# Optimization experiments

Measured on AMD Instinct MI355X. Metric: run time of the kernel, lower is better.

Reference implementation:

```python
import jax, jax.numpy as jnp
import numpy as np

EPS = 1e-5  # BatchNorm eps

def _bn(x):
    # BatchNorm1d(affine=False) in training mode: per-agent, per-feature batch stats
    m = jnp.mean(x, axis=1, keepdims=True)
    v = jnp.var(x, axis=1, keepdims=True)
    return (x - m) / jnp.sqrt(v + EPS)

def _lrelu(x):
    return jax.nn.leaky_relu(x, 0.01)

def setup_inputs() -> dict:
    key = jax.random.key(0)
    ks = jax.random.split(key, 14)
    A, B, IN, OUT, H, K = 8, 32768, 128, 32, 128, 4
    D = H // K
    s = 0.05
    return {
        "states": jax.random.normal(ks[0], (A, B, IN), jnp.float32),
        "actions": jax.random.normal(ks[1], (A, B, OUT), jnp.float32),
        "enc_w": jax.random.normal(ks[2], (A, IN + OUT, H), jnp.float32) * s,
        "enc_b": jax.random.normal(ks[3], (A, H), jnp.float32) * s,
        "aenc_w": jax.random.normal(ks[4], (A, OUT, H), jnp.float32) * s,
        "aenc_b": jax.random.normal(ks[5], (A, H), jnp.float32) * s,
        "key_w": jax.random.normal(ks[6], (K, H, D), jnp.float32) * s,
        "sel_w": jax.random.normal(ks[7], (K, H, D), jnp.float32) * s,
        "val_w": jax.random.normal(ks[8], (K, H, D), jnp.float32) * s,
        "val_b": jax.random.normal(ks[9], (K, D), jnp.float32) * s,
        "c1_w": jax.random.normal(ks[10], (A, 2 * H, H), jnp.float32) * s,
        "c1_b": jax.random.normal(ks[11], (A, H), jnp.float32) * s,
        "c2_w": jax.random.normal(ks[12], (A, H, 1), jnp.float32) * s,
        "c2_b": jax.random.normal(ks[13], (A, 1), jnp.float32) * s,
    }

def reference(states, actions, enc_w, enc_b, aenc_w, aenc_b,
              key_w, sel_w, val_w, val_b, c1_w, c1_b, c2_w, c2_b):
    A, B, _ = states.shape
    # per-agent state-action encodings: [A,B,H]
    sa = _bn(jnp.concatenate([states, actions], axis=-1))
    sa_enc = _lrelu(jnp.einsum('abi,aih->abh', sa, enc_w) + enc_b[:, None, :])
    # per-agent action encodings: [A,B,H]
    a_in = _bn(actions)
    a_enc = _lrelu(jnp.einsum('abi,aih->abh', a_in, aenc_w) + aenc_b[:, None, :])
    # per-head keys/values/selectors: [K,A,B,D]
    keys = jnp.einsum('abh,khd->kabd', a_enc, key_w)
    vals = _lrelu(jnp.einsum('abh,khd->kabd', a_enc, val_w) + val_b[:, None, None, :])
    sels = jnp.einsum('abh,khd->kabd', sa_enc, sel_w)
    D = keys.shape[-1]
    # attention logits over other agents: [K,B,A_query,A_key], self excluded
    logits = jnp.einsum('kibd,kjbd->kbij', sels, keys) / jnp.sqrt(jnp.float32(D))
    self_mask = jnp.eye(A, dtype=bool)[None, None]
    probs = jax.nn.softmax(jnp.where(self_mask, -jnp.inf, logits), axis=-1)
    # attended values: [K,A,B,D] -> concat heads -> [A,B,K*D]
    other = jnp.einsum('kbij,kjbd->kibd', probs, vals)
    other_cat = jnp.transpose(other, (1, 2, 0, 3)).reshape(A, B, -1)
    # per-agent critics on [sa_enc, attended]: [A,B,1]
    critic_in = jnp.concatenate([sa_enc, other_cat], axis=-1)
    h = _lrelu(jnp.einsum('abi,aih->abh', critic_in, c1_w) + c1_b[:, None, :])
    q = jnp.einsum('abh,aho->abo', h, c2_w) + c2_b[:, None, :]
    return q
```

## Files before the change

kernel.cpp:

```cpp
#include <hip/hip_runtime.h>
#include <hip/hip_bf16.h>
#include <stdint.h>

#define A_N 8
#define B_N 32768
#define IN_N 128
#define OUT_N 32
#define SAF 160
#define H_N 128
#define D_N 32
#define KD_N 128
#define CIN_N 256
#define CHUNKS 128
#define EPSV 1e-5f
#define ENC_KP 192

typedef unsigned int u32;
typedef unsigned short u16;
typedef __attribute__((ext_vector_type(8))) short short8;
typedef __attribute__((ext_vector_type(4))) float floatx4;

__device__ __forceinline__ float bf_lo(u32 u){ return __uint_as_float(u << 16); }
__device__ __forceinline__ float bf_hi(u32 u){ return __uint_as_float(u & 0xffff0000u); }
__device__ __forceinline__ float bf2f(u16 b){ return __uint_as_float(((u32)b) << 16); }
__device__ __forceinline__ u16 f2bf(float f){
  u32 u = __float_as_uint(f);
  return (u16)((u + 0x7fffu + ((u >> 16) & 1u)) >> 16);
}
__device__ __forceinline__ float lrelu(float x){ return x > 0.f ? x : 0.01f * x; }

__global__ __launch_bounds__(256) void k_stats(
    const float* __restrict__ states, const float* __restrict__ actions,
    float* __restrict__ part)
{
  int a = blockIdx.y;
  int chunk = blockIdx.x;
  int t = threadIdx.x;
  int r0 = chunk * (B_N / CHUNKS);
  __shared__ float red[512];
  {
    int f = t & 127, half = t >> 7;
    const float* p = states + ((size_t)a * B_N + r0 + half) * IN_N + f;
    float s1 = 0.f, s2 = 0.f;
    for (int it = 0; it < 128; ++it){
      float v = p[(size_t)(2 * it) * IN_N];
      s1 += v; s2 += v * v;
    }
    red[t] = s1; red[256 + t] = s2;
    __syncthreads();
    if (t < 128){
      float a1 = red[t] + red[t + 128];
      float a2 = red[256 + t] + red[256 + t + 128];
      size_t o = (((size_t)a * CHUNKS + chunk) * SAF + t) * 2;
      part[o] = a1; part[o + 1] = a2;
    }
    __syncthreads();
  }
  {
    int f = t & 31, g = t >> 5;
    const float* p = actions + ((size_t)a * B_N + r0 + g) * OUT_N + f;
    float s1 = 0.f, s2 = 0.f;
    for (int it = 0; it < 32; ++it){
      float v = p[(size_t)(8 * it) * OUT_N];
      s1 += v; s2 += v * v;
    }
    red[t] = s1; red[256 + t] = s2;
    __syncthreads();
    if (t < 32){
      float a1 = 0.f, a2 = 0.f;
      #pragma unroll
      for (int gg = 0; gg < 8; ++gg){
        a1 += red[t + 32 * gg];
        a2 += red[256 + t + 32 * gg];
      }
      size_t o = (((size_t)a * CHUNKS + chunk) * SAF + 128 + t) * 2;
      part[o] = a1; part[o + 1] = a2;
    }
  }
}

__global__ void k_finalize(const float* __restrict__ part,
                           float* __restrict__ meanArr, float* __restrict__ istdArr)
{
  int idx = blockIdx.x * blockDim.x + threadIdx.x;
  if (idx >= A_N * SAF) return;
  int a = idx / SAF, f = idx % SAF;
  float s1 = 0.f, s2 = 0.f;
  for (int c = 0; c < CHUNKS; ++c){
    size_t o = (((size_t)a * CHUNKS + c) * SAF + f) * 2;
    s1 += part[o]; s2 += part[o + 1];
  }
  float m = s1 * (1.f / B_N);
  float v = s2 * (1.f / B_N) - m * m;
  if (v < 0.f) v = 0.f;
  meanArr[idx] = m;
  istdArr[idx] = rsqrtf(v + EPSV);
}

__device__ __forceinline__ void packpair(float w, u16* __restrict__ dh,
                                         u16* __restrict__ dl, int i){
  u16 h = f2bf(w);
  dh[i] = h;
  dl[i] = f2bf(w - bf2f(h));
}

__global__ __launch_bounds__(256) void k_pack(
    const float* __restrict__ enc_w, const float* __restrict__ aenc_w,
    const float* __restrict__ key_w, const float* __restrict__ sel_w,
    const float* __restrict__ val_w, const float* __restrict__ c1_w,
    u16* __restrict__ encH, u16* __restrict__ encL,
    u16* __restrict__ aencH, u16* __restrict__ aencL,
    u16* __restrict__ keyH, u16* __restrict__ keyL,
    u16* __restrict__ selH, u16* __restrict__ selL,
    u16* __restrict__ valH, u16* __restrict__ valL,
    u16* __restrict__ c1H, u16* __restrict__ c1L)
{
  int i = blockIdx.x * 256 + threadIdx.x;
  const int S0 = A_N * H_N * ENC_KP;
  const int S1 = A_N * H_N * OUT_N;
  const int S2 = KD_N * H_N;
  const int S5 = A_N * H_N * CIN_N;
  if (i < S0){
    int a = i / (H_N * ENC_KP); int r = i % (H_N * ENC_KP);
    int n = r / ENC_KP; int k = r % ENC_KP;
    float v = (k < SAF) ? enc_w[((size_t)a * SAF + k) * H_N + n] : 0.f;
    packpair(v, encH, encL, i);
    return;
  }
  i -= S0;
  if (i < S1){
    int a = i / (H_N * OUT_N); int r = i % (H_N * OUT_N);
    int n = r / OUT_N; int k = r % OUT_N;
    packpair(aenc_w[((size_t)a * OUT_N + k) * H_N + n], aencH, aencL, i);
    return;
  }
  i -= S1;
  if (i < 3 * S2){
    int which = i / S2; int j = i % S2;
    int n = j / H_N, k = j % H_N;
    const float* w = (which == 0) ? key_w : ((which == 1) ? sel_w : val_w);
    u16* dh = (which == 0) ? keyH : ((which == 1) ? selH : valH);
    u16* dl = (which == 0) ? keyL : ((which == 1) ? selL : valL);
    packpair(w[(((size_t)(n >> 5)) * H_N + k) * D_N + (n & 31)], dh, dl, j);
    return;
  }
  i -= 3 * S2;
  if (i < S5){
    int a = i / (H_N * CIN_N); int r = i % (H_N * CIN_N);
    int n = r / CIN_N; int k = r % CIN_N;
    packpair(c1_w[((size_t)a * CIN_N + k) * H_N + n], c1H, c1L, i);
  }
}
#define PACK_TOTAL (A_N*H_N*ENC_KP + A_N*H_N*OUT_N + 3*KD_N*H_N + A_N*H_N*CIN_N)

__global__ __launch_bounds__(256, 2) void k_enc_sel(
    const float* __restrict__ states, const float* __restrict__ actions,
    const float* __restrict__ mean, const float* __restrict__ istd,
    const u16* __restrict__ encH, const u16* __restrict__ encL,
    const float* __restrict__ enc_b,
    const u16* __restrict__ selH, const u16* __restrict__ selL,
    u16* __restrict__ sa_enc, u16* __restrict__ sels)
{
  int a = blockIdx.y; int row0 = blockIdx.x * 128; int t = threadIdx.x;
  int lane = t & 63, wave = t >> 6, l16 = lane & 15, quad = lane >> 4;
  __shared__ __align__(16) u16 WA[18432];
  __shared__ __align__(16) u16 XA[18432];
  __shared__ __align__(16) float sc[192], sh[192];
  u16* Wh = WA; u16* Wl = WA + 9216;
  u16* Xh = XA; u16* Xl = XA + 9216;
  u16* T  = XA;

  if (t < 192){
    float m = 0.f, s = 0.f;
    if (t < SAF){ m = mean[a * SAF + t]; s = istd[a * SAF + t]; }
    sc[t] = s; sh[t] = -m * s;
  }
  floatx4 acc[2][8];
  #pragma unroll
  for (int mt = 0; mt < 2; ++mt)
    #pragma unroll
    for (int nt = 0; nt < 8; ++nt) acc[mt][nt] = (floatx4){0.f,0.f,0.f,0.f};
  const u16* wbh = encH + (size_t)a * H_N * ENC_KP;
  const u16* wbl = encL + (size_t)a * H_N * ENC_KP;
  __syncthreads();

  for (int k0 = 0; k0 < ENC_KP; k0 += 64){
    for (int c = t; c < 1024; c += 256){
      int n = c >> 3, off = (c & 7) * 8;
      *(uint4*)&Wh[n * 72 + off] = *(const uint4*)(wbh + (size_t)n * ENC_KP + k0 + off);
      *(uint4*)&Wl[n * 72 + off] = *(const uint4*)(wbl + (size_t)n * ENC_KP + k0 + off);
    }
    for (int c = t; c < 2048; c += 256){
      int r = c >> 4, kc = (c & 15) * 4, f = k0 + kc;
      size_t row = (size_t)a * B_N + row0 + r;
      float4 v = {0.f, 0.f, 0.f, 0.f};
      if (f < IN_N)     v = *(const float4*)(states + row * IN_N + f);
      else if (f < SAF) v = *(const float4*)(actions + row * OUT_N + (f - IN_N));
      float4 scv = *(const float4*)&sc[f];
      float4 shv = *(const float4*)&sh[f];
      float x0 = fmaf(v.x, scv.x, shv.x), x1 = fmaf(v.y, scv.y, shv.y);
      float x2 = fmaf(v.z, scv.z, shv.z), x3 = fmaf(v.w, scv.w, shv.w);
      u16 h0 = f2bf(x0), h1 = f2bf(x1), h2 = f2bf(x2), h3 = f2bf(x3);
      *(u32*)&Xh[r * 72 + kc]     = (u32)h0 | ((u32)h1 << 16);
      *(u32*)&Xh[r * 72 + kc + 2] = (u32)h2 | ((u32)h3 << 16);
      u16 l0 = f2bf(x0 - bf2f(h0)), l1 = f2bf(x1 - bf2f(h1));
      u16 l2 = f2bf(x2 - bf2f(h2)), l3 = f2bf(x3 - bf2f(h3));
      *(u32*)&Xl[r * 72 + kc]     = (u32)l0 | ((u32)l1 << 16);
      *(u32*)&Xl[r * 72 + kc + 2] = (u32)l2 | ((u32)l3 << 16);
    }
    __syncthreads();
    #pragma unroll
    for (int ks = 0; ks < 64; ks += 32){
      short8 ah[2], al[2], bh[8], bl[8];
      #pragma unroll
      for (int mt = 0; mt < 2; ++mt){
        int rr = (wave * 32 + mt * 16 + l16) * 72 + ks + quad * 8;
        ah[mt] = *(const short8*)&Xh[rr];
        al[mt] = *(const short8*)&Xl[rr];
      }
      #pragma unroll
      for (int nt = 0; nt < 8; ++nt){
        int rr = (nt * 16 + l16) * 72 + ks + quad * 8;
        bh[nt] = *(const short8*)&Wh[rr];
        bl[nt] = *(const short8*)&Wl[rr];
      }
      #pragma unroll
      for (int mt = 0; mt < 2; ++mt)
        #pragma unroll
        for (int nt = 0; nt < 8; ++nt){
          acc[mt][nt] = __builtin_amdgcn_mfma_f32_16x16x32_bf16(ah[mt], bh[nt], acc[mt][nt], 0,0,0);
          acc[mt][nt] = __builtin_amdgcn_mfma_f32_16x16x32_bf16(ah[mt], bl[nt], acc[mt][nt], 0,0,0);
          acc[mt][nt] = __builtin_amdgcn_mfma_f32_16x16x32_bf16(al[mt], bh[nt], acc[mt][nt], 0,0,0);
        }
    }
    __syncthreads();
  }

  {
    float bv[8];
    #pragma unroll
    for (int nt = 0; nt < 8; ++nt) bv[nt] = enc_b[a * H_N + nt * 16 + l16];
    #pragma unroll
    for (int mt = 0; mt < 2; ++mt)
      #pragma unroll
      for (int nt = 0; nt < 8; ++nt)
        #pragma unroll
        for (int r = 0; r < 4; ++r){
          int rl = wave * 32 + mt * 16 + quad * 4 + r;
          T[rl * 136 + nt * 16 + l16] = f2bf(lrelu(acc[mt][nt][r] + bv[nt]));
        }
  }
  __syncthreads();
  for (int c = t; c < 2048; c += 256){
    int row = c >> 4, col8 = (c & 15) * 8;
    *(uint4*)(sa_enc + ((size_t)a * B_N + row0 + row) * H_N + col8) =
        *(const uint4*)&T[row * 136 + col8];
  }

  #pragma unroll
  for (int mt = 0; mt < 2; ++mt)
    #pragma unroll
    for (int nt = 0; nt < 8; ++nt) acc[mt][nt] = (floatx4){0.f,0.f,0.f,0.f};
  for (int k0 = 0; k0 < H_N; k0 += 64){
    __syncthreads();
    for (int c = t; c < 1024; c += 256){
      int n = c >> 3, off = (c & 7) * 8;
      *(uint4*)&Wh[n * 72 + off] = *(const uint4*)(selH + (size_t)n * H_N + k0 + off);
      *(uint4*)&Wl[n * 72 + off] = *(const uint4*)(selL + (size_t)n * H_N + k0 + off);
    }
    __syncthreads();
    #pragma unroll
    for (int ks = 0; ks < 64; ks += 32){
      short8 ah[2], bh[8], bl[8];
      #pragma unroll
      for (int mt = 0; mt < 2; ++mt)
        ah[mt] = *(const short8*)&T[(wave * 32 + mt * 16 + l16) * 136 + k0 + ks + quad * 8];
      #pragma unroll
      for (int nt = 0; nt < 8; ++nt){
        int rr = (nt * 16 + l16) * 72 + ks + quad * 8;
        bh[nt] = *(const short8*)&Wh[rr];
        bl[nt] = *(const short8*)&Wl[rr];
      }
      #pragma unroll
      for (int mt = 0; mt < 2; ++mt)
        #pragma unroll
        for (int nt = 0; nt < 8; ++nt){
          acc[mt][nt] = __builtin_amdgcn_mfma_f32_16x16x32_bf16(ah[mt], bh[nt], acc[mt][nt], 0,0,0);
          acc[mt][nt] = __builtin_amdgcn_mfma_f32_16x16x32_bf16(ah[mt], bl[nt], acc[mt][nt], 0,0,0);
        }
    }
  }
  __syncthreads();
  #pragma unroll
  for (int mt = 0; mt < 2; ++mt)
    #pragma unroll
    for (int nt = 0; nt < 8; ++nt)
      #pragma unroll
      for (int r = 0; r < 4; ++r){
        int rl = wave * 32 + mt * 16 + quad * 4 + r;
        T[rl * 136 + nt * 16 + l16] = f2bf(acc[mt][nt][r]);
      }
  __syncthreads();
  for (int c = t; c < 2048; c += 256){
    int row = c >> 4, col8 = (c & 15) * 8;
    *(uint4*)(sels + ((size_t)a * B_N + row0 + row) * H_N + col8) =
        *(const uint4*)&T[row * 136 + col8];
  }
}

__global__ __launch_bounds__(256, 2) void k_aenc_kv(
    const float* __restrict__ actions,
    const float* __restrict__ mean, const float* __restrict__ istd,
    const u16* __restrict__ aencH, const u16* __restrict__ aencL,
    const float* __restrict__ aenc_b,
    const u16* __restrict__ keyH, const u16* __restrict__ keyL,
    const u16* __restrict__ valH, const u16* __restrict__ valL,
    const float* __restrict__ val_b,
    u16* __restrict__ keys, u16* __restrict__ vals)
{
  int a = blockIdx.y; int row0 = blockIdx.x * 128; int t = threadIdx.x;
  int lane = t & 63, wave = t >> 6, l16 = lane & 15, quad = lane >> 4;
  __shared__ __align__(16) u16 WA[18432];
  __shared__ __align__(16) u16 TA[17408];
  __shared__ __align__(16) float sc[32], sh[32];
  u16* T = TA;

  if (t < 32){
    float m = mean[a * SAF + 128 + t], s = istd[a * SAF + 128 + t];
    sc[t] = s; sh[t] = -m * s;
  }
  floatx4 acc[2][8];
  #pragma unroll
  for (int mt = 0; mt < 2; ++mt)
    #pragma unroll
    for (int nt = 0; nt < 8; ++nt) acc[mt][nt] = (floatx4){0.f,0.f,0.f,0.f};
  __syncthreads();

  {
    u16* Xh = TA; u16* Xl = TA + 5120;
    u16* Wh1 = WA; u16* Wl1 = WA + 5120;
    const u16* wbh = aencH + (size_t)a * H_N * OUT_N;
    const u16* wbl = aencL + (size_t)a * H_N * OUT_N;
    for (int c = t; c < 512; c += 256){
      int n = c >> 2, off = (c & 3) * 8;
      *(uint4*)&Wh1[n * 40 + off] = *(const uint4*)(wbh + (size_t)n * OUT_N + off);
      *(uint4*)&Wl1[n * 40 + off] = *(const uint4*)(wbl + (size_t)n * OUT_N + off);
    }
    for (int c = t; c < 1024; c += 256){
      int r = c >> 3, kc = (c & 7) * 4;
      size_t row = (size_t)a * B_N + row0 + r;
      float4 v = *(const float4*)(actions + row * OUT_N + kc);
      float4 scv = *(const float4*)&sc[kc];
      float4 shv = *(const float4*)&sh[kc];
      float x0 = fmaf(v.x, scv.x, shv.x), x1 = fmaf(v.y, scv.y, shv.y);
      float x2 = fmaf(v.z, scv.z, shv.z), x3 = fmaf(v.w, scv.w, shv.w);
      u16 h0 = f2bf(x0), h1 = f2bf(x1), h2 = f2bf(x2), h3 = f2bf(x3);
      *(u32*)&Xh[r * 40 + kc]     = (u32)h0 | ((u32)h1 << 16);
      *(u32*)&Xh[r * 40 + kc + 2] = (u32)h2 | ((u32)h3 << 16);
      u16 l0 = f2bf(x0 - bf2f(h0)), l1 = f2bf(x1 - bf2f(h1));
      u16 l2 = f2bf(x2 - bf2f(h2)), l3 = f2bf(x3 - bf2f(h3));
      *(u32*)&Xl[r * 40 + kc]     = (u32)l0 | ((u32)l1 << 16);
      *(u32*)&Xl[r * 40 + kc + 2] = (u32)l2 | ((u32)l3 << 16);
    }
    __syncthreads();
    short8 ah[2], al[2], bh[8], bl[8];
    #pragma unroll
    for (int mt = 0; mt < 2; ++mt){
      int rr = (wave * 32 + mt * 16 + l16) * 40 + quad * 8;
      ah[mt] = *(const short8*)&Xh[rr];
      al[mt] = *(const short8*)&Xl[rr];
    }
    #pragma unroll
    for (int nt = 0; nt < 8; ++nt){
      int rr = (nt * 16 + l16) * 40 + quad * 8;
      bh[nt] = *(const short8*)&Wh1[rr];
      bl[nt] = *(const short8*)&Wl1[rr];
    }
    #pragma unroll
    for (int mt = 0; mt < 2; ++mt)
      #pragma unroll
      for (int nt = 0; nt < 8; ++nt){
        acc[mt][nt] = __builtin_amdgcn_mfma_f32_16x16x32_bf16(ah[mt], bh[nt], acc[mt][nt], 0,0,0);
        acc[mt][nt] = __builtin_amdgcn_mfma_f32_16x16x32_bf16(ah[mt], bl[nt], acc[mt][nt], 0,0,0);
        acc[mt][nt] = __builtin_amdgcn_mfma_f32_16x16x32_bf16(al[mt], bh[nt], acc[mt][nt], 0,0,0);
      }
    __syncthreads();
  }
  {
    float bv[8];
    #pragma unroll
    for (int nt = 0; nt < 8; ++nt) bv[nt] = aenc_b[a * H_N + nt * 16 + l16];
    #pragma unroll
    for (int mt = 0; mt < 2; ++mt)
      #pragma unroll
      for (int nt = 0; nt < 8; ++nt)
        #pragma unroll
        for (int r = 0; r < 4; ++r){
          int rl = wave * 32 + mt * 16 + quad * 4 + r;
          T[rl * 136 + nt * 16 + l16] = f2bf(lrelu(acc[mt][nt][r] + bv[nt]));
        }
  }

  u16* Wh = WA; u16* Wl = WA + 9216;
  #pragma unroll
  for (int mt = 0; mt < 2; ++mt)
    #pragma unroll
    for (int nt = 0; nt < 8; ++nt) acc[mt][nt] = (floatx4){0.f,0.f,0.f,0.f};
  for (int k0 = 0; k0 < H_N; k0 += 64){
    __syncthreads();
    for (int c = t; c < 1024; c += 256){
      int n = c >> 3, off = (c & 7) * 8;
      *(uint4*)&Wh[n * 72 + off] = *(const uint4*)(keyH + (size_t)n * H_N + k0 + off);
      *(uint4*)&Wl[n * 72 + off] = *(const uint4*)(keyL + (size_t)n * H_N + k0 + off);
    }
    __syncthreads();
    #pragma unroll
    for (int ks = 0; ks < 64; ks += 32){
      short8 ah[2], bh[8], bl[8];
      #pragma unroll
      for (int mt = 0; mt < 2; ++mt)
        ah[mt] = *(const short8*)&T[(wave * 32 + mt * 16 + l16) * 136 + k0 + ks + quad * 8];
      #pragma unroll
      for (int nt = 0; nt < 8; ++nt){
        int rr = (nt * 16 + l16) * 72 + ks + quad * 8;
        bh[nt] = *(const short8*)&Wh[rr];
        bl[nt] = *(const short8*)&Wl[rr];
      }
      #pragma unroll
      for (int mt = 0; mt < 2; ++mt)
        #pragma unroll
        for (int nt = 0; nt < 8; ++nt){
          acc[mt][nt] = __builtin_amdgcn_mfma_f32_16x16x32_bf16(ah[mt], bh[nt], acc[mt][nt], 0,0,0);
          acc[mt][nt] = __builtin_amdgcn_mfma_f32_16x16x32_bf16(ah[mt], bl[nt], acc[mt][nt], 0,0,0);
        }
    }
  }
  #pragma unroll
  for (int mt = 0; mt < 2; ++mt)
    #pragma unroll
    for (int nt = 0; nt < 8; ++nt)
      #pragma unroll
      for (int r = 0; r < 4; ++r){
        int rl = wave * 32 + mt * 16 + quad * 4 + r;
        keys[((size_t)a * B_N + row0 + rl) * H_N + nt * 16 + l16] = f2bf(acc[mt][nt][r]);
      }

  #pragma unroll
  for (int mt = 0; mt < 2; ++mt)
    #pragma unroll
    for (int nt = 0; nt < 8; ++nt) acc[mt][nt] = (floatx4){0.f,0.f,0.f,0.f};
  for (int k0 = 0; k0 < H_N; k0 += 64){
    __syncthreads();
    for (int c = t; c < 1024; c += 256){
      int n = c >> 3, off = (c & 7) * 8;
      *(uint4*)&Wh[n * 72 + off] = *(const uint4*)(valH + (size_t)n * H_N + k0 + off);
      *(uint4*)&Wl[n * 72 + off] = *(const uint4*)(valL + (size_t)n * H_N + k0 + off);
    }
    __syncthreads();
    #pragma unroll
    for (int ks = 0; ks < 64; ks += 32){
      short8 ah[2], bh[8], bl[8];
      #pragma unroll
      for (int mt = 0; mt < 2; ++mt)
        ah[mt] = *(const short8*)&T[(wave * 32 + mt * 16 + l16) * 136 + k0 + ks + quad * 8];
      #pragma unroll
      for (int nt = 0; nt < 8; ++nt){
        int rr = (nt * 16 + l16) * 72 + ks + quad * 8;
        bh[nt] = *(const short8*)&Wh[rr];
        bl[nt] = *(const short8*)&Wl[rr];
      }
      #pragma unroll
      for (int mt = 0; mt < 2; ++mt)
        #pragma unroll
        for (int nt = 0; nt < 8; ++nt){
          acc[mt][nt] = __builtin_amdgcn_mfma_f32_16x16x32_bf16(ah[mt], bh[nt], acc[mt][nt], 0,0,0);
          acc[mt][nt] = __builtin_amdgcn_mfma_f32_16x16x32_bf16(ah[mt], bl[nt], acc[mt][nt], 0,0,0);
        }
    }
  }
  __syncthreads();
  {
    float bv[8];
    #pragma unroll
    for (int nt = 0; nt < 8; ++nt) bv[nt] = val_b[nt * 16 + l16];
    #pragma unroll
    for (int mt = 0; mt < 2; ++mt)
      #pragma unroll
      for (int nt = 0; nt < 8; ++nt)
        #pragma unroll
        for (int r = 0; r < 4; ++r){
          int rl = wave * 32 + mt * 16 + quad * 4 + r;
          T[rl * 136 + nt * 16 + l16] = f2bf(lrelu(acc[mt][nt][r] + bv[nt]));
        }
  }
  __syncthreads();
  for (int c = t; c < 2048; c += 256){
    int row = c >> 4, col8 = (c & 15) * 8;
    *(uint4*)(vals + ((size_t)a * B_N + row0 + row) * H_N + col8) =
        *(const uint4*)&T[row * 136 + col8];
  }
}

__global__ __launch_bounds__(256) void k_attn(
    const u16* __restrict__ sels, const u16* __restrict__ keys,
    const u16* __restrict__ vals, u16* __restrict__ other)
{
  int b0 = blockIdx.x * 8;
  int t = threadIdx.x;
  __shared__ __align__(16) u16 sS[8192], sK[8192], sV[8192];
  u32* dS = (u32*)sS; u32* dK = (u32*)sK; u32* dV = (u32*)sV;
  #pragma unroll
  for (int a = 0; a < 8; ++a){
    size_t go = ((size_t)a * B_N + b0) * KD_N;
    const u32* gs = (const u32*)(sels + go);
    const u32* gk = (const u32*)(keys + go);
    const u32* gv = (const u32*)(vals + go);
    dS[a * 512 + t] = gs[t]; dS[a * 512 + 256 + t] = gs[256 + t];
    dK[a * 512 + t] = gk[t]; dK[a * 512 + 256 + t] = gk[256 + t];
    dV[a * 512 + t] = gv[t]; dV[a * 512 + 256 + t] = gv[256 + t];
  }
  __syncthreads();
  int i = t & 7, p = t >> 3;
  int k = p & 3, bl = p >> 2;
  int base_i = (i * 8 + bl) * 128 + k * 32;
  float si[32];
  {
    const u32* S32 = (const u32*)&sS[base_i];
    #pragma unroll
    for (int d2 = 0; d2 < 16; ++d2){
      u32 u = S32[d2];
      si[2 * d2] = bf_lo(u); si[2 * d2 + 1] = bf_hi(u);
    }
  }
  float lg[8];
  #pragma unroll
  for (int j = 0; j < 8; ++j){
    const u32* K32 = (const u32*)&sK[(j * 8 + bl) * 128 + k * 32];
    float acc = 0.f;
    #pragma unroll
    for (int d2 = 0; d2 < 16; ++d2){
      u32 u = K32[d2];
      acc = fmaf(si[2 * d2], bf_lo(u), acc);
      acc = fmaf(si[2 * d2 + 1], bf_hi(u), acc);
    }
    lg[j] = acc * 0.17677669529663689f;
  }
  float mx = -3.0e38f;
  #pragma unroll
  for (int j = 0; j < 8; ++j) if (j != i) mx = fmaxf(mx, lg[j]);
  float pe[8], se = 0.f;
  #pragma unroll
  for (int j = 0; j < 8; ++j){
    pe[j] = (j == i) ? 0.f : __expf(lg[j] - mx);
    se += pe[j];
  }
  float inv = 1.f / se;
  #pragma unroll
  for (int j = 0; j < 8; ++j) pe[j] *= inv;
  __align__(16) u16 ob[32];
  #pragma unroll
  for (int d2 = 0; d2 < 16; ++d2){
    float acc0 = 0.f, acc1 = 0.f;
    #pragma unroll
    for (int j = 0; j < 8; ++j){
      u32 u = *(const u32*)&sV[(j * 8 + bl) * 128 + k * 32 + 2 * d2];
      acc0 = fmaf(pe[j], bf_lo(u), acc0);
      acc1 = fmaf(pe[j], bf_hi(u), acc1);
    }
    ob[2 * d2] = f2bf(acc0); ob[2 * d2 + 1] = f2bf(acc1);
  }
  uint4* dst = (uint4*)(other + ((size_t)i * B_N + (b0 + bl)) * KD_N + k * 32);
  const uint4* s4 = (const uint4*)ob;
  #pragma unroll
  for (int c = 0; c < 4; ++c) dst[c] = s4[c];
}

__global__ __launch_bounds__(256, 2) void k_critic(
    const u16* __restrict__ sa_enc, const u16* __restrict__ other,
    const u16* __restrict__ c1H, const u16* __restrict__ c1L,
    const float* __restrict__ c1_b,
    const float* __restrict__ c2w, const float* __restrict__ c2b,
    float* __restrict__ qout)
{
  int a = blockIdx.y; int row0 = blockIdx.x * 128; int t = threadIdx.x;
  int lane = t & 63, wave = t >> 6, l16 = lane & 15, quad = lane >> 4;
  __shared__ __align__(16) u16 Xs[9216];
  __shared__ __align__(16) u16 Wh[9216];
  __shared__ __align__(16) u16 Wl[9216];
  floatx4 acc[2][8];
  #pragma unroll
  for (int mt = 0; mt < 2; ++mt)
    #pragma unroll
    for (int nt = 0; nt < 8; ++nt) acc[mt][nt] = (floatx4){0.f,0.f,0.f,0.f};
  const u16* wbh = c1H + (size_t)a * H_N * CIN_N;
  const u16* wbl = c1L + (size_t)a * H_N * CIN_N;

  for (int k0 = 0; k0 < CIN_N; k0 += 64){
    for (int c = t; c < 1024; c += 256){
      int n = c >> 3, off = (c & 7) * 8;
      *(uint4*)&Wh[n * 72 + off] = *(const uint4*)(wbh + (size_t)n * CIN_N + k0 + off);
      *(uint4*)&Wl[n * 72 + off] = *(const uint4*)(wbl + (size_t)n * CIN_N + k0 + off);
    }
    for (int c = t; c < 1024; c += 256){
      int r = c >> 3, off = (c & 7) * 8;
      int fo = k0 + off;
      const u16* src = sa_enc;
      if (fo >= H_N){ src = other; fo -= H_N; }
      *(uint4*)&Xs[r * 72 + off] =
          *(const uint4*)(src + ((size_t)a * B_N + row0 + r) * H_N + fo);
    }
    __syncthreads();
    #pragma unroll
    for (int ks = 0; ks < 64; ks += 32){
      short8 ah[2], bh[8], bl[8];
      #pragma unroll
      for (int mt = 0; mt < 2; ++mt)
        ah[mt] = *(const short8*)&Xs[(wave * 32 + mt * 16 + l16) * 72 + ks + quad * 8];
      #pragma unroll
      for (int nt = 0; nt < 8; ++nt){
        int rr = (nt * 16 + l16) * 72 + ks + quad * 8;
        bh[nt] = *(const short8*)&Wh[rr];
        bl[nt] = *(const short8*)&Wl[rr];
      }
      #pragma unroll
      for (int mt = 0; mt < 2; ++mt)
        #pragma unroll
        for (int nt = 0; nt < 8; ++nt){
          acc[mt][nt] = __builtin_amdgcn_mfma_f32_16x16x32_bf16(ah[mt], bh[nt], acc[mt][nt], 0,0,0);
          acc[mt][nt] = __builtin_amdgcn_mfma_f32_16x16x32_bf16(ah[mt], bl[nt], acc[mt][nt], 0,0,0);
        }
    }
    __syncthreads();
  }

  float c2r[8], bv[8];
  #pragma unroll
  for (int nt = 0; nt < 8; ++nt){
    c2r[nt] = c2w[a * H_N + nt * 16 + l16];
    bv[nt]  = c1_b[a * H_N + nt * 16 + l16];
  }
  #pragma unroll
  for (int mt = 0; mt < 2; ++mt){
    #pragma unroll
    for (int r = 0; r < 4; ++r){
      float s = 0.f;
      #pragma unroll
      for (int nt = 0; nt < 8; ++nt){
        float h = lrelu(acc[mt][nt][r] + bv[nt]);
        s = fmaf(h, c2r[nt], s);
      }
      s += __shfl_xor(s, 1);
      s += __shfl_xor(s, 2);
      s += __shfl_xor(s, 4);
      s += __shfl_xor(s, 8);
      if (l16 == 0){
        int row = row0 + wave * 32 + mt * 16 + quad * 4 + r;
        qout[(size_t)a * B_N + row] = s + c2b[a];
      }
    }
  }
}

extern "C" void kernel_launch(void* const* d_in, const int* in_sizes, int n_in,
                              void* d_out, int out_size, void* d_ws, size_t ws_size,
                              hipStream_t stream)
{
  const float* states  = (const float*)d_in[0];
  const float* actions = (const float*)d_in[1];
  const float* enc_w   = (const float*)d_in[2];
  const float* enc_b   = (const float*)d_in[3];
  const float* aenc_w  = (const float*)d_in[4];
  const float* aenc_b  = (const float*)d_in[5];
  const float* key_w   = (const float*)d_in[6];
  const float* sel_w   = (const float*)d_in[7];
  const float* val_w   = (const float*)d_in[8];
  const float* val_b   = (const float*)d_in[9];
  const float* c1_w    = (const float*)d_in[10];
  const float* c1_b    = (const float*)d_in[11];
  const float* c2_w    = (const float*)d_in[12];
  const float* c2_b    = (const float*)d_in[13];
  float* q = (float*)d_out;

  char* ws = (char*)d_ws;
  u16* encH  = (u16*)(ws + 0);
  u16* encL  = (u16*)(ws + 393216);
  u16* aencH = (u16*)(ws + 786432);
  u16* aencL = (u16*)(ws + 851968);
  u16* keyH  = (u16*)(ws + 917504);
  u16* keyL  = (u16*)(ws + 950272);
  u16* selH  = (u16*)(ws + 983040);
  u16* selL  = (u16*)(ws + 1015808);
  u16* valH  = (u16*)(ws + 1048576);
  u16* valL  = (u16*)(ws + 1081344);
  float* part    = (float*)ws;
  float* meanArr = (float*)(ws + 1310720);
  float* istdArr = (float*)(ws + 1315840);
  u16* c1H = (u16*)(ws + 1320960);
  u16* c1L = (u16*)(ws + 1845248);
  const size_t ibase = 4194304;
  const size_t BUF = (size_t)A_N * B_N * 128 * 2;
  u16* sa_enc = (u16*)(ws + ibase);
  u16* sels   = (u16*)(ws + ibase + BUF);
  u16* keys   = (u16*)(ws + ibase + 2 * BUF);
  u16* vals   = (u16*)(ws + ibase + 3 * BUF);

  k_stats<<<dim3(CHUNKS, A_N), 256, 0, stream>>>(states, actions, part);
  k_finalize<<<(A_N * SAF + 255) / 256, 256, 0, stream>>>(part, meanArr, istdArr);
  k_pack<<<(PACK_TOTAL + 255) / 256, 256, 0, stream>>>(
      enc_w, aenc_w, key_w, sel_w, val_w, c1_w,
      encH, encL, aencH, aencL, keyH, keyL, selH, selL, valH, valL, c1H, c1L);

  dim3 g(B_N / 128, A_N);
  k_enc_sel<<<g, 256, 0, stream>>>(states, actions, meanArr, istdArr,
                                   encH, encL, enc_b, selH, selL, sa_enc, sels);
  k_aenc_kv<<<g, 256, 0, stream>>>(actions, meanArr, istdArr,
                                   aencH, aencL, aenc_b, keyH, keyL,
                                   valH, valL, val_b, keys, vals);
  k_attn<<<B_N / 8, 256, 0, stream>>>(sels, keys, vals, keys);
  k_critic<<<g, 256, 0, stream>>>(sa_enc, keys, c1H, c1L, c1_b, c2_w, c2_b, q);
}
```

Before: 599.5 us.

## Drop low-half weights for key/sel/val, fuse key+val GEMMs, shrink LDS tiles

The key, selector and value projection weights now use a single bf16 copy instead of a hi/lo split, which halves their MFMA count and weight traffic. The key and value projections in k_aenc_kv are fused into one K-loop with two accumulator sets that share the A-operand loads. In k_enc_sel and k_critic the K-tile shrinks from 64 to 32 to cut LDS use, and launch bounds rise to allow 3 blocks per CU. The cost is lower precision on those projections, more barriers per K step, and more register pressure from the dual accumulators.

```diff
diff --git a/kernel.cpp b/kernel.cpp
--- a/kernel.cpp
+++ b/kernel.cpp
@@ -110,9 +110,7 @@
     const float* __restrict__ val_w, const float* __restrict__ c1_w,
     u16* __restrict__ encH, u16* __restrict__ encL,
     u16* __restrict__ aencH, u16* __restrict__ aencL,
-    u16* __restrict__ keyH, u16* __restrict__ keyL,
-    u16* __restrict__ selH, u16* __restrict__ selL,
-    u16* __restrict__ valH, u16* __restrict__ valL,
+    u16* __restrict__ keyH, u16* __restrict__ selH, u16* __restrict__ valH,
     u16* __restrict__ c1H, u16* __restrict__ c1L)
 {
   int i = blockIdx.x * 256 + threadIdx.x;
@@ -140,8 +138,7 @@
     int n = j / H_N, k = j % H_N;
     const float* w = (which == 0) ? key_w : ((which == 1) ? sel_w : val_w);
     u16* dh = (which == 0) ? keyH : ((which == 1) ? selH : valH);
-    u16* dl = (which == 0) ? keyL : ((which == 1) ? selL : valL);
-    packpair(w[(((size_t)(n >> 5)) * H_N + k) * D_N + (n & 31)], dh, dl, j);
+    dh[j] = f2bf(w[(((size_t)(n >> 5)) * H_N + k) * D_N + (n & 31)]);
     return;
   }
   i -= 3 * S2;
@@ -153,22 +150,24 @@
 }
 #define PACK_TOTAL (A_N*H_N*ENC_KP + A_N*H_N*OUT_N + 3*KD_N*H_N + A_N*H_N*CIN_N)
 
-__global__ __launch_bounds__(256, 2) void k_enc_sel(
+__global__ __launch_bounds__(256, 3) void k_enc_sel(
     const float* __restrict__ states, const float* __restrict__ actions,
     const float* __restrict__ mean, const float* __restrict__ istd,
     const u16* __restrict__ encH, const u16* __restrict__ encL,
     const float* __restrict__ enc_b,
-    const u16* __restrict__ selH, const u16* __restrict__ selL,
+    const u16* __restrict__ selH,
     u16* __restrict__ sa_enc, u16* __restrict__ sels)
 {
   int a = blockIdx.y; int row0 = blockIdx.x * 128; int t = threadIdx.x;
   int lane = t & 63, wave = t >> 6, l16 = lane & 15, quad = lane >> 4;
-  __shared__ __align__(16) u16 WA[18432];
-  __shared__ __align__(16) u16 XA[18432];
+  __shared__ __align__(16) u16 S[22528];
   __shared__ __align__(16) float sc[192], sh[192];
-  u16* Wh = WA; u16* Wl = WA + 9216;
-  u16* Xh = XA; u16* Xl = XA + 9216;
-  u16* T  = XA;
+  u16* Wh = S;
+  u16* Wl = S + 5120;
+  u16* Xh = S + 10240;
+  u16* Xl = S + 15360;
+  u16* T  = S;
+  u16* Ws = S + 17408;
 
   if (t < 192){
     float m = 0.f, s = 0.f;
@@ -184,14 +183,14 @@
   const u16* wbl = encL + (size_t)a * H_N * ENC_KP;
   __syncthreads();
 
-  for (int k0 = 0; k0 < ENC_KP; k0 += 64){
+  for (int k0 = 0; k0 < ENC_KP; k0 += 32){
+    for (int c = t; c < 512; c += 256){
+      int n = c >> 2, off = (c & 3) * 8;
+      *(uint4*)&Wh[n * 40 + off] = *(const uint4*)(wbh + (size_t)n * ENC_KP + k0 + off);
+      *(uint4*)&Wl[n * 40 + off] = *(const uint4*)(wbl + (size_t)n * ENC_KP + k0 + off);
+    }
     for (int c = t; c < 1024; c += 256){
-      int n = c >> 3, off = (c & 7) * 8;
-      *(uint4*)&Wh[n * 72 + off] = *(const uint4*)(wbh + (size_t)n * ENC_KP + k0 + off);
-      *(uint4*)&Wl[n * 72 + off] = *(const uint4*)(wbl + (size_t)n * ENC_KP + k0 + off);
-    }
-    for (int c = t; c < 2048; c += 256){
-      int r = c >> 4, kc = (c & 15) * 4, f = k0 + kc;
+      int r = c >> 3, kc = (c & 7) * 4, f = k0 + kc;
       size_t row = (size_t)a * B_N + row0 + r;
       float4 v = {0.f, 0.f, 0.f, 0.f};
       if (f < IN_N)     v = *(const float4*)(states + row * IN_N + f);
@@ -201,26 +200,25 @@
       float x0 = fmaf(v.x, scv.x, shv.x), x1 = fmaf(v.y, scv.y, shv.y);
       float x2 = fmaf(v.z, scv.z, shv.z), x3 = fmaf(v.w, scv.w, shv.w);
       u16 h0 = f2bf(x0), h1 = f2bf(x1), h2 = f2bf(x2), h3 = f2bf(x3);
-      *(u32*)&Xh[r * 72 + kc]     = (u32)h0 | ((u32)h1 << 16);
-      *(u32*)&Xh[r * 72 + kc + 2] = (u32)h2 | ((u32)h3 << 16);
+      *(u32*)&Xh[r * 40 + kc]     = (u32)h0 | ((u32)h1 << 16);
+      *(u32*)&Xh[r * 40 + kc + 2] = (u32)h2 | ((u32)h3 << 16);
       u16 l0 = f2bf(x0 - bf2f(h0)), l1 = f2bf(x1 - bf2f(h1));
       u16 l2 = f2bf(x2 - bf2f(h2)), l3 = f2bf(x3 - bf2f(h3));
-      *(u32*)&Xl[r * 72 + kc]     = (u32)l0 | ((u32)l1 << 16);
-      *(u32*)&Xl[r * 72 + kc + 2] = (u32)l2 | ((u32)l3 << 16);
-    }
-    __syncthreads();
-    #pragma unroll
-    for (int ks = 0; ks < 64; ks += 32){
+      *(u32*)&Xl[r * 40 + kc]     = (u32)l0 | ((u32)l1 << 16);
+      *(u32*)&Xl[r * 40 + kc + 2] = (u32)l2 | ((u32)l3 << 16);
+    }
+    __syncthreads();
+    {
       short8 ah[2], al[2], bh[8], bl[8];
       #pragma unroll
       for (int mt = 0; mt < 2; ++mt){
-        int rr = (wave * 32 + mt * 16 + l16) * 72 + ks + quad * 8;
+        int rr = (wave * 32 + mt * 16 + l16) * 40 + quad * 8;
         ah[mt] = *(const short8*)&Xh[rr];
         al[mt] = *(const short8*)&Xl[rr];
       }
       #pragma unroll
       for (int nt = 0; nt < 8; ++nt){
-        int rr = (nt * 16 + l16) * 72 + ks + quad * 8;
+        int rr = (nt * 16 + l16) * 40 + quad * 8;
         bh[nt] = *(const short8*)&Wh[rr];
         bl[nt] = *(const short8*)&Wl[rr];
       }
@@ -261,36 +259,28 @@
   for (int mt = 0; mt < 2; ++mt)
     #pragma unroll
     for (int nt = 0; nt < 8; ++nt) acc[mt][nt] = (floatx4){0.f,0.f,0.f,0.f};
-  for (int k0 = 0; k0 < H_N; k0 += 64){
-    __syncthreads();
-    for (int c = t; c < 1024; c += 256){
-      int n = c >> 3, off = (c & 7) * 8;
-      *(uint4*)&Wh[n * 72 + off] = *(const uint4*)(selH + (size_t)n * H_N + k0 + off);
-      *(uint4*)&Wl[n * 72 + off] = *(const uint4*)(selL + (size_t)n * H_N + k0 + off);
-    }
-    __syncthreads();
-    #pragma unroll
-    for (int ks = 0; ks < 64; ks += 32){
-      short8 ah[2], bh[8], bl[8];
+  for (int k0 = 0; k0 < H_N; k0 += 32){
+    for (int c = t; c < 512; c += 256){
+      int n = c >> 2, off = (c & 3) * 8;
+      *(uint4*)&Ws[n * 40 + off] = *(const uint4*)(selH + (size_t)n * H_N + k0 + off);
+    }
+    __syncthreads();
+    {
+      short8 ah[2], bh[8];
       #pragma unroll
       for (int mt = 0; mt < 2; ++mt)
-        ah[mt] = *(const short8*)&T[(wave * 32 + mt * 16 + l16) * 136 + k0 + ks + quad * 8];
-      #pragma unroll
-      for (int nt = 0; nt < 8; ++nt){
-        int rr = (nt * 16 + l16) * 72 + ks + quad * 8;
-        bh[nt] = *(const short8*)&Wh[rr];
-        bl[nt] = *(const short8*)&Wl[rr];
-      }
+        ah[mt] = *(const short8*)&T[(wave * 32 + mt * 16 + l16) * 136 + k0 + quad * 8];
+      #pragma unroll
+      for (int nt = 0; nt < 8; ++nt)
+        bh[nt] = *(const short8*)&Ws[(nt * 16 + l16) * 40 + quad * 8];
       #pragma unroll
       for (int mt = 0; mt < 2; ++mt)
         #pragma unroll
-        for (int nt = 0; nt < 8; ++nt){
+        for (int nt = 0; nt < 8; ++nt)
           acc[mt][nt] = __builtin_amdgcn_mfma_f32_16x16x32_bf16(ah[mt], bh[nt], acc[mt][nt], 0,0,0);
-          acc[mt][nt] = __builtin_amdgcn_mfma_f32_16x16x32_bf16(ah[mt], bl[nt], acc[mt][nt], 0,0,0);
-        }
-    }
-  }
-  __syncthreads();
+    }
+    __syncthreads();
+  }
   #pragma unroll
   for (int mt = 0; mt < 2; ++mt)
     #pragma unroll
@@ -313,32 +303,36 @@
     const float* __restrict__ mean, const float* __restrict__ istd,
     const u16* __restrict__ aencH, const u16* __restrict__ aencL,
     const float* __restrict__ aenc_b,
-    const u16* __restrict__ keyH, const u16* __restrict__ keyL,
-    const u16* __restrict__ valH, const u16* __restrict__ valL,
+    const u16* __restrict__ keyH, const u16* __restrict__ valH,
     const float* __restrict__ val_b,
     u16* __restrict__ keys, u16* __restrict__ vals)
 {
   int a = blockIdx.y; int row0 = blockIdx.x * 128; int t = threadIdx.x;
   int lane = t & 63, wave = t >> 6, l16 = lane & 15, quad = lane >> 4;
-  __shared__ __align__(16) u16 WA[18432];
-  __shared__ __align__(16) u16 TA[17408];
+  __shared__ __align__(16) u16 S[35840];
   __shared__ __align__(16) float sc[32], sh[32];
-  u16* T = TA;
+  u16* T  = S;
+  u16* WK = S + 17408;
+  u16* WV = S + 26624;
+  u16* T2 = S + 17408;
 
   if (t < 32){
     float m = mean[a * SAF + 128 + t], s = istd[a * SAF + 128 + t];
     sc[t] = s; sh[t] = -m * s;
   }
-  floatx4 acc[2][8];
+  floatx4 accK[2][8], accV[2][8];
   #pragma unroll
   for (int mt = 0; mt < 2; ++mt)
     #pragma unroll
-    for (int nt = 0; nt < 8; ++nt) acc[mt][nt] = (floatx4){0.f,0.f,0.f,0.f};
+    for (int nt = 0; nt < 8; ++nt){
+      accK[mt][nt] = (floatx4){0.f,0.f,0.f,0.f};
+      accV[mt][nt] = (floatx4){0.f,0.f,0.f,0.f};
+    }
   __syncthreads();
 
   {
-    u16* Xh = TA; u16* Xl = TA + 5120;
-    u16* Wh1 = WA; u16* Wl1 = WA + 5120;
+    u16* Wh1 = S;  u16* Wl1 = S + 5120;
+    u16* Xh = S + 10240; u16* Xl = S + 15360;
     const u16* wbh = aencH + (size_t)a * H_N * OUT_N;
     const u16* wbl = aencL + (size_t)a * H_N * OUT_N;
     for (int c = t; c < 512; c += 256){
@@ -380,9 +374,9 @@
     for (int mt = 0; mt < 2; ++mt)
       #pragma unroll
       for (int nt = 0; nt < 8; ++nt){
-        acc[mt][nt] = __builtin_amdgcn_mfma_f32_16x16x32_bf16(ah[mt], bh[nt], acc[mt][nt], 0,0,0);
-        acc[mt][nt] = __builtin_amdgcn_mfma_f32_16x16x32_bf16(ah[mt], bl[nt], acc[mt][nt], 0,0,0);
-        acc[mt][nt] = __builtin_amdgcn_mfma_f32_16x16x32_bf16(al[mt], bh[nt], acc[mt][nt], 0,0,0);
+        accK[mt][nt] = __builtin_amdgcn_mfma_f32_16x16x32_bf16(ah[mt], bh[nt], accK[mt][nt], 0,0,0);
+        accK[mt][nt] = __builtin_amdgcn_mfma_f32_16x16x32_bf16(ah[mt], bl[nt], accK[mt][nt], 0,0,0);
+        accK[mt][nt] = __builtin_amdgcn_mfma_f32_16x16x32_bf16(al[mt], bh[nt], accK[mt][nt], 0,0,0);
       }
     __syncthreads();
   }
@@ -390,6 +384,53 @@
     float bv[8];
     #pragma unroll
     for (int nt = 0; nt < 8; ++nt) bv[nt] = aenc_b[a * H_N + nt * 16 + l16];
+    #pragma unroll
+    for (int mt = 0; mt < 2; ++mt)
+      #pragma unroll
+      for (int nt = 0; nt < 8; ++nt){
+        #pragma unroll
+        for (int r = 0; r < 4; ++r){
+          int rl = wave * 32 + mt * 16 + quad * 4 + r;
+          T[rl * 136 + nt * 16 + l16] = f2bf(lrelu(accK[mt][nt][r] + bv[nt]));
+        }
+        accK[mt][nt] = (floatx4){0.f,0.f,0.f,0.f};
+      }
+  }
+
+  for (int k0 = 0; k0 < H_N; k0 += 64){
+    __syncthreads();
+    for (int c = t; c < 1024; c += 256){
+      int n = c >> 3, off = (c & 7) * 8;
+      *(uint4*)&WK[n * 72 + off] = *(const uint4*)(keyH + (size_t)n * H_N + k0 + off);
+      *(uint4*)&WV[n * 72 + off] = *(const uint4*)(valH + (size_t)n * H_N + k0 + off);
+    }
+    __syncthreads();
+    #pragma unroll
+    for (int ks = 0; ks < 64; ks += 32){
+      short8 ah[2], bk[8], bv[8];
+      #pragma unroll
+      for (int mt = 0; mt < 2; ++mt)
+        ah[mt] = *(const short8*)&T[(wave * 32 + mt * 16 + l16) * 136 + k0 + ks + quad * 8];
+      #pragma unroll
+      for (int nt = 0; nt < 8; ++nt){
+        int rr = (nt * 16 + l16) * 72 + ks + quad * 8;
+        bk[nt] = *(const short8*)&WK[rr];
+        bv[nt] = *(const short8*)&WV[rr];
+      }
+      #pragma unroll
+      for (int mt = 0; mt < 2; ++mt)
+        #pragma unroll
+        for (int nt = 0; nt < 8; ++nt){
+          accK[mt][nt] = __builtin_amdgcn_mfma_f32_16x16x32_bf16(ah[mt], bk[nt], accK[mt][nt], 0,0,0);
+          accV[mt][nt] = __builtin_amdgcn_mfma_f32_16x16x32_bf16(ah[mt], bv[nt], accV[mt][nt], 0,0,0);
+        }
+    }
+  }
+  __syncthreads();
+  {
+    float bv[8];
+    #pragma unroll
+    for (int nt = 0; nt < 8; ++nt) bv[nt] = val_b[nt * 16 + l16];
     #pragma unroll
     for (int mt = 0; mt < 2; ++mt)
       #pragma unroll
@@ -397,100 +438,8 @@
         #pragma unroll
         for (int r = 0; r < 4; ++r){
           int rl = wave * 32 + mt * 16 + quad * 4 + r;
-          T[rl * 136 + nt * 16 + l16] = f2bf(lrelu(acc[mt][nt][r] + bv[nt]));
-        }
-  }
-
-  u16* Wh = WA; u16* Wl = WA + 9216;
-  #pragma unroll
-  for (int mt = 0; mt < 2; ++mt)
-    #pragma unroll
-    for (int nt = 0; nt < 8; ++nt) acc[mt][nt] = (floatx4){0.f,0.f,0.f,0.f};
-  for (int k0 = 0; k0 < H_N; k0 += 64){
-    __syncthreads();
-    for (int c = t; c < 1024; c += 256){
-      int n = c >> 3, off = (c & 7) * 8;
-      *(uint4*)&Wh[n * 72 + off] = *(const uint4*)(keyH + (size_t)n * H_N + k0 + off);
-      *(uint4*)&Wl[n * 72 + off] = *(const uint4*)(keyL + (size_t)n * H_N + k0 + off);
-    }
-    __syncthreads();
-    #pragma unroll
-    for (int ks = 0; ks < 64; ks += 32){
-      short8 ah[2], bh[8], bl[8];
-      #pragma unroll
-      for (int mt = 0; mt < 2; ++mt)
-        ah[mt] = *(const short8*)&T[(wave * 32 + mt * 16 + l16) * 136 + k0 + ks + quad * 8];
-      #pragma unroll
-      for (int nt = 0; nt < 8; ++nt){
-        int rr = (nt * 16 + l16) * 72 + ks + quad * 8;
-        bh[nt] = *(const short8*)&Wh[rr];
-        bl[nt] = *(const short8*)&Wl[rr];
-      }
-      #pragma unroll
-      for (int mt = 0; mt < 2; ++mt)
-        #pragma unroll
-        for (int nt = 0; nt < 8; ++nt){
-          acc[mt][nt] = __builtin_amdgcn_mfma_f32_16x16x32_bf16(ah[mt], bh[nt], acc[mt][nt], 0,0,0);
-          acc[mt][nt] = __builtin_amdgcn_mfma_f32_16x16x32_bf16(ah[mt], bl[nt], acc[mt][nt], 0,0,0);
-        }
-    }
-  }
-  #pragma unroll
-  for (int mt = 0; mt < 2; ++mt)
-    #pragma unroll
-    for (int nt = 0; nt < 8; ++nt)
-      #pragma unroll
-      for (int r = 0; r < 4; ++r){
-        int rl = wave * 32 + mt * 16 + quad * 4 + r;
-        keys[((size_t)a * B_N + row0 + rl) * H_N + nt * 16 + l16] = f2bf(acc[mt][nt][r]);
-      }
-
-  #pragma unroll
-  for (int mt = 0; mt < 2; ++mt)
-    #pragma unroll
-    for (int nt = 0; nt < 8; ++nt) acc[mt][nt] = (floatx4){0.f,0.f,0.f,0.f};
-  for (int k0 = 0; k0 < H_N; k0 += 64){
-    __syncthreads();
-    for (int c = t; c < 1024; c += 256){
-      int n = c >> 3, off = (c & 7) * 8;
-      *(uint4*)&Wh[n * 72 + off] = *(const uint4*)(valH + (size_t)n * H_N + k0 + off);
-      *(uint4*)&Wl[n * 72 + off] = *(const uint4*)(valL + (size_t)n * H_N + k0 + off);
-    }
-    __syncthreads();
-    #pragma unroll
-    for (int ks = 0; ks < 64; ks += 32){
-      short8 ah[2], bh[8], bl[8];
-      #pragma unroll
-      for (int mt = 0; mt < 2; ++mt)
-        ah[mt] = *(const short8*)&T[(wave * 32 + mt * 16 + l16) * 136 + k0 + ks + quad * 8];
-      #pragma unroll
-      for (int nt = 0; nt < 8; ++nt){
-        int rr = (nt * 16 + l16) * 72 + ks + quad * 8;
-        bh[nt] = *(const short8*)&Wh[rr];
-        bl[nt] = *(const short8*)&Wl[rr];
-      }
-      #pragma unroll
-      for (int mt = 0; mt < 2; ++mt)
-        #pragma unroll
-        for (int nt = 0; nt < 8; ++nt){
-          acc[mt][nt] = __builtin_amdgcn_mfma_f32_16x16x32_bf16(ah[mt], bh[nt], acc[mt][nt], 0,0,0);
-          acc[mt][nt] = __builtin_amdgcn_mfma_f32_16x16x32_bf16(ah[mt], bl[nt], acc[mt][nt], 0,0,0);
-        }
-    }
-  }
-  __syncthreads();
-  {
-    float bv[8];
-    #pragma unroll
-    for (int nt = 0; nt < 8; ++nt) bv[nt] = val_b[nt * 16 + l16];
-    #pragma unroll
-    for (int mt = 0; mt < 2; ++mt)
-      #pragma unroll
-      for (int nt = 0; nt < 8; ++nt)
-        #pragma unroll
-        for (int r = 0; r < 4; ++r){
-          int rl = wave * 32 + mt * 16 + quad * 4 + r;
-          T[rl * 136 + nt * 16 + l16] = f2bf(lrelu(acc[mt][nt][r] + bv[nt]));
+          T[rl * 136 + nt * 16 + l16]  = f2bf(lrelu(accV[mt][nt][r] + bv[nt]));
+          T2[rl * 136 + nt * 16 + l16] = f2bf(accK[mt][nt][r]);
         }
   }
   __syncthreads();
@@ -498,6 +447,8 @@
     int row = c >> 4, col8 = (c & 15) * 8;
     *(uint4*)(vals + ((size_t)a * B_N + row0 + row) * H_N + col8) =
         *(const uint4*)&T[row * 136 + col8];
+    *(uint4*)(keys + ((size_t)a * B_N + row0 + row) * H_N + col8) =
+        *(const uint4*)&T2[row * 136 + col8];
   }
 }
 
@@ -575,7 +526,7 @@
   for (int c = 0; c < 4; ++c) dst[c] = s4[c];
 }
 
-__global__ __launch_bounds__(256, 2) void k_critic(
+__global__ __launch_bounds__(256, 3) void k_critic(
     const u16* __restrict__ sa_enc, const u16* __restrict__ other,
     const u16* __restrict__ c1H, const u16* __restrict__ c1L,
     const float* __restrict__ c1_b,
@@ -584,9 +535,9 @@
 {
   int a = blockIdx.y; int row0 = blockIdx.x * 128; int t = threadIdx.x;
   int lane = t & 63, wave = t >> 6, l16 = lane & 15, quad = lane >> 4;
-  __shared__ __align__(16) u16 Xs[9216];
-  __shared__ __align__(16) u16 Wh[9216];
-  __shared__ __align__(16) u16 Wl[9216];
+  __shared__ __align__(16) u16 Xs[5120];
+  __shared__ __align__(16) u16 Wh[5120];
+  __shared__ __align__(16) u16 Wl[5120];
   floatx4 acc[2][8];
   #pragma unroll
   for (int mt = 0; mt < 2; ++mt)
@@ -595,30 +546,29 @@
   const u16* wbh = c1H + (size_t)a * H_N * CIN_N;
   const u16* wbl = c1L + (size_t)a * H_N * CIN_N;
 
-  for (int k0 = 0; k0 < CIN_N; k0 += 64){
-    for (int c = t; c < 1024; c += 256){
-      int n = c >> 3, off = (c & 7) * 8;
-      *(uint4*)&Wh[n * 72 + off] = *(const uint4*)(wbh + (size_t)n * CIN_N + k0 + off);
-      *(uint4*)&Wl[n * 72 + off] = *(const uint4*)(wbl + (size_t)n * CIN_N + k0 + off);
-    }
-    for (int c = t; c < 1024; c += 256){
-      int r = c >> 3, off = (c & 7) * 8;
+  for (int k0 = 0; k0 < CIN_N; k0 += 32){
+    for (int c = t; c < 512; c += 256){
+      int n = c >> 2, off = (c & 3) * 8;
+      *(uint4*)&Wh[n * 40 + off] = *(const uint4*)(wbh + (size_t)n * CIN_N + k0 + off);
+      *(uint4*)&Wl[n * 40 + off] = *(const uint4*)(wbl + (size_t)n * CIN_N + k0 + off);
+    }
+    for (int c = t; c < 512; c += 256){
+      int r = c >> 2, off = (c & 3) * 8;
       int fo = k0 + off;
       const u16* src = sa_enc;
       if (fo >= H_N){ src = other; fo -= H_N; }
-      *(uint4*)&Xs[r * 72 + off] =
+      *(uint4*)&Xs[r * 40 + off] =
           *(const uint4*)(src + ((size_t)a * B_N + row0 + r) * H_N + fo);
     }
     __syncthreads();
-    #pragma unroll
-    for (int ks = 0; ks < 64; ks += 32){
+    {
       short8 ah[2], bh[8], bl[8];
       #pragma unroll
       for (int mt = 0; mt < 2; ++mt)
-        ah[mt] = *(const short8*)&Xs[(wave * 32 + mt * 16 + l16) * 72 + ks + quad * 8];
+        ah[mt] = *(const short8*)&Xs[(wave * 32 + mt * 16 + l16) * 40 + quad * 8];
       #pragma unroll
       for (int nt = 0; nt < 8; ++nt){
-        int rr = (nt * 16 + l16) * 72 + ks + quad * 8;
+        int rr = (nt * 16 + l16) * 40 + quad * 8;
         bh[nt] = *(const short8*)&Wh[rr];
         bl[nt] = *(const short8*)&Wl[rr];
       }
@@ -687,11 +637,8 @@
   u16* aencH = (u16*)(ws + 786432);
   u16* aencL = (u16*)(ws + 851968);
   u16* keyH  = (u16*)(ws + 917504);
-  u16* keyL  = (u16*)(ws + 950272);
-  u16* selH  = (u16*)(ws + 983040);
-  u16* selL  = (u16*)(ws + 1015808);
-  u16* valH  = (u16*)(ws + 1048576);
-  u16* valL  = (u16*)(ws + 1081344);
+  u16* selH  = (u16*)(ws + 950272);
+  u16* valH  = (u16*)(ws + 983040);
   float* part    = (float*)ws;
   float* meanArr = (float*)(ws + 1310720);
   float* istdArr = (float*)(ws + 1315840);
@@ -708,14 +655,14 @@
   k_finalize<<<(A_N * SAF + 255) / 256, 256, 0, stream>>>(part, meanArr, istdArr);
   k_pack<<<(PACK_TOTAL + 255) / 256, 256, 0, stream>>>(
       enc_w, aenc_w, key_w, sel_w, val_w, c1_w,
-      encH, encL, aencH, aencL, keyH, keyL, selH, selL, valH, valL, c1H, c1L);
+      encH, encL, aencH, aencL, keyH, selH, valH, c1H, c1L);
 
   dim3 g(B_N / 128, A_N);
   k_enc_sel<<<g, 256, 0, stream>>>(states, actions, meanArr, istdArr,
-                                   encH, encL, enc_b, selH, selL, sa_enc, sels);
+                                   encH, encL, enc_b, selH, sa_enc, sels);
   k_aenc_kv<<<g, 256, 0, stream>>>(actions, meanArr, istdArr,
-                                   aencH, aencL, aenc_b, keyH, keyL,
-                                   valH, valL, val_b, keys, vals);
+                                   aencH, aencL, aenc_b, keyH, valH, val_b,
+                                   keys, vals);
   k_attn<<<B_N / 8, 256, 0, stream>>>(sels, keys, vals, keys);
   k_critic<<<g, 256, 0, stream>>>(sa_enc, keys, c1H, c1L, c1_b, c2_w, c2_b, q);
 }
```

New measurement: 543.3 us. -9.4%, faster.
